# Optimization experiments

Measured on AMD Instinct MI355X. Metric: run time of the kernel, lower is better.

The kernel has to match this reference:

```python
import jax, jax.numpy as jnp
import numpy as np

N, D, DIN, S, R = 128, 2560, 5120, 16, 160  # users, d_model, d_inner, d_state, dt_rank


def setup_inputs() -> dict:
    key = jax.random.key(0)
    ks = jax.random.split(key, 16)
    f = lambda k, shape, s: jax.random.normal(k, shape, dtype=jnp.float32) * s
    return {
        "x": f(ks[0], (1, 1, N, D), 1.0),
        "conv_state0": f(ks[1], (1, 1, N, DIN), 0.1),
        "conv_state1": f(ks[2], (1, 1, N, DIN), 0.1),
        "conv_state2": f(ks[3], (1, 1, N, DIN), 0.1),
        "conv_state3": f(ks[4], (1, 1, N, DIN), 0.1),
        "ssm_state": f(ks[5], (N, DIN, S), 0.1),
        "ssm_proj": f(ks[6], (D, DIN), 0.02),
        "mlp_proj": f(ks[7], (D, DIN), 0.02),
        "down_proj": f(ks[8], (DIN, D), 0.02),
        "conv_w": f(ks[9], (4, DIN), 0.2),
        "conv_bias": f(ks[10], (DIN,), 0.1),
        "x_proj_w": f(ks[11], (DIN, R + 2 * S), 0.02),
        "dt_proj_w": f(ks[12], (R, DIN), 0.05),
        "dt_proj_b": f(ks[13], (DIN,), 0.1),
        "A_log": jnp.log(jnp.broadcast_to(jnp.arange(1, S + 1, dtype=jnp.float32), (DIN, S))),
        "D_param": jnp.ones((DIN,), jnp.float32),
    }


def reference(x, conv_state0, conv_state1, conv_state2, conv_state3, ssm_state,
              ssm_proj, mlp_proj, down_proj, conv_w, conv_bias,
              x_proj_w, dt_proj_w, dt_proj_b, A_log, D_param):
    r = dt_proj_w.shape[0]
    s = A_log.shape[1]
    x2 = x[0, 0]                         # (N, D)
    xs = x2 @ ssm_proj                   # (N, DIN) in_proj (ssm half)
    # shifted conv state window: oldest state (conv_state0) is dropped
    states = (conv_state1[0, 0], conv_state2[0, 0], conv_state3[0, 0], xs)
    conv_out = conv_bias + conv_w[0] * states[0] + conv_w[1] * states[1] \
        + conv_w[2] * states[2] + conv_w[3] * states[3]   # (N, DIN)
    u = jax.nn.silu(conv_out)
    # selective-scan single step (TtMambaSSM)
    proj = u @ x_proj_w                  # (N, R + 2S)
    dt = jax.nn.softplus(proj[:, :r] @ dt_proj_w + dt_proj_b)  # (N, DIN)
    Bm = proj[:, r:r + s]                # (N, S)
    Cm = proj[:, r + s:]                 # (N, S)
    A = -jnp.exp(A_log)                  # (DIN, S)
    dA = jnp.exp(dt[:, :, None] * A[None])                     # (N, DIN, S)
    h = dA * ssm_state + dt[:, :, None] * Bm[:, None, :] * u[:, :, None]
    y = jnp.einsum('nds,ns->nd', h, Cm) + D_param * u          # (N, DIN)
    # residual/gate branch and output projection (note: no silu on res, as in source)
    res = x2 @ mlp_proj                  # (N, DIN)
    out = (y * res) @ down_proj          # (N, D)
    return out[None, None]               # (1, 1, N, D)
```

## Files before the change

kernel.cpp:

```cpp
#include <hip/hip_runtime.h>

using u16 = unsigned short;
using u32 = unsigned int;

typedef __attribute__((ext_vector_type(8))) short short8;
typedef __attribute__((ext_vector_type(4))) float floatx4;

constexpr int TOKENS = 128;
constexpr int DM = 2560;
constexpr int DI = 5120;
constexpr int NS = 16;
constexpr int NR = 160;
constexpr int NP = 192;

constexpr size_t ND    = (size_t)TOKENS * DI;
constexpr size_t XS_P  = 0;
constexpr size_t RES_P = XS_P + 8 * ND;
constexpr size_t U_OFF = RES_P + 8 * ND;
constexpr size_t DT_P  = U_OFF + ND;
constexpr size_t PRJ_P = DT_P + 5 * ND;
constexpr size_t PRJ   = PRJ_P + 40 * (size_t)(TOKENS * NP);
constexpr size_t NEED  = PRJ + (size_t)(TOKENS * NP);

constexpr size_t S_XS  = 0;
constexpr size_t S_RES = S_XS + ND;
constexpr size_t S_U   = S_RES + ND;
constexpr size_t S_DT  = S_U + ND;
constexpr size_t S_PRJ = S_DT + ND;
constexpr size_t S_OAC = S_PRJ + (size_t)(TOKENS * NP);

__device__ __forceinline__ float bf2f(u16 h) {
  u32 u = ((u32)h) << 16;
  return __builtin_bit_cast(float, u);
}
__device__ __forceinline__ u16 f2bf(float f) {
  u32 u = __builtin_bit_cast(u32, f);
  u += 0x7FFFu + ((u >> 16) & 1u);
  return (u16)(u >> 16);
}
__device__ __forceinline__ u32 pk2(float a, float b) {
  u32 r;
  asm("v_cvt_pk_bf16_f32 %0, %1, %2" : "=v"(r) : "v"(a), "v"(b));
  return r;
}
__device__ __forceinline__ float ldsc(const void* p, size_t i, bool bf) {
  return bf ? bf2f(((const u16*)p)[i]) : ((const float*)p)[i];
}
__device__ __forceinline__ uint4 ld8(const void* p, size_t i, bool bf) {
  if (bf) return *(const uint4*)((const u16*)p + i);
  const float4* f = (const float4*)((const float*)p + i);
  float4 a = f[0], b = f[1];
  return (uint4){pk2(a.x, a.y), pk2(a.z, a.w), pk2(b.x, b.y), pk2(b.z, b.w)};
}
__device__ __forceinline__ void ld8f(const void* p, size_t i, bool bf, float* o) {
  if (bf) {
    uint4 v = *(const uint4*)((const u16*)p + i);
    const u16* h = (const u16*)&v;
#pragma unroll
    for (int e = 0; e < 8; e++) o[e] = bf2f(h[e]);
  } else {
    const float4* f = (const float4*)((const float*)p + i);
    float4 a = f[0], b = f[1];
    o[0] = a.x; o[1] = a.y; o[2] = a.z; o[3] = a.w;
    o[4] = b.x; o[5] = b.y; o[6] = b.z; o[7] = b.w;
  }
}

struct GemmP {
  const void* A; int lda; int a_ws;
  const void* B; const void* B2;
  float* C; float* C2;
  int ldb; int ldc;
  int ksteps;
  int nx_half;
  int atomic;
  size_t cstride;
  const u32* probe;
};

__global__ __launch_bounds__(256, 4) void gemm_k(GemmP p) {
  __shared__ __align__(16) u16 As[128 * 32];
  __shared__ __align__(16) u16 Bs[64 * 32];

  const bool bf = (p.probe[0] != 0u);
  const int tid = threadIdx.x;
  const int bx = blockIdx.x;
  const void* B = p.B; float* C = p.C;
  int nblk = bx;
  if (bx >= p.nx_half) { B = p.B2; C = p.C2; nblk = bx - p.nx_half; }
  const int n0 = nblk * 64;
  const int kstart = blockIdx.y * p.ksteps * 32;
  if (!p.atomic) C += blockIdx.y * p.cstride;

  const int wave = tid >> 6, lane = tid & 63;
  const int q = lane >> 4, l16 = lane & 15;
  const int wx = wave & 1, wy = wave >> 1;

  const bool a_f32 = p.a_ws || !bf;

  const int ac = tid & 3;
  const int am0 = tid >> 2;
  const bool bact = tid < 128;
  const int bc = tid & 7, pr = (tid >> 3) & 15;
  const int bn8 = bc * 8, k2 = 2 * pr;

  floatx4 acc[4][2];
#pragma unroll
  for (int mi = 0; mi < 4; mi++)
#pragma unroll
    for (int ni = 0; ni < 2; ni++) acc[mi][ni] = (floatx4){0.f, 0.f, 0.f, 0.f};

  auto load_tiles = [&](int ks, uint4* aO, uint4* bO) {
    const int kb = kstart + ks * 32;
#pragma unroll
    for (int pa = 0; pa < 2; pa++) {
      const int m = am0 + pa * 64;
      const size_t off = (size_t)m * p.lda + kb + ac * 8;
      if (!a_f32) {
        aO[pa] = *(const uint4*)((const u16*)p.A + off);
      } else {
        const float4* f = (const float4*)((const float*)p.A + off);
        float4 x0 = f[0], x1 = f[1];
        aO[pa] = (uint4){pk2(x0.x, x0.y), pk2(x0.z, x0.w),
                         pk2(x1.x, x1.y), pk2(x1.z, x1.w)};
      }
    }
    if (bact) {
      bO[0] = ld8(B, (size_t)(kb + k2) * p.ldb + n0 + bn8, bf);
      bO[1] = ld8(B, (size_t)(kb + k2 + 1) * p.ldb + n0 + bn8, bf);
    }
  };

  auto store_tiles = [&](const uint4* aO, const uint4* bO) {
#pragma unroll
    for (int pa = 0; pa < 2; pa++) {
      const int m = am0 + pa * 64;
      *(uint4*)&As[m * 32 + ((ac ^ (m & 3)) << 3)] = aO[pa];
    }
    if (bact) {
      const u16* lo = (const u16*)&bO[0];
      const u16* hi = (const u16*)&bO[1];
#pragma unroll
      for (int j = 0; j < 8; j++) {
        const int n = bn8 + j;
        const int blk = (k2 >> 3) ^ ((n ^ (n >> 3)) & 3);
        *(u32*)&Bs[n * 32 + (blk << 3) + (k2 & 7)] =
            (u32)lo[j] | ((u32)hi[j] << 16);
      }
    }
  };

  const int swA = l16 & 3;
  const int arow = (wy * 64 + l16) * 32;
  const int ao = ((q ^ swA) << 3);
  int nrow[2], bo[2];
#pragma unroll
  for (int ni = 0; ni < 2; ni++) {
    const int n = wx * 32 + ni * 16 + l16;
    nrow[ni] = n * 32;
    bo[ni] = ((q ^ ((n ^ (n >> 3)) & 3)) << 3);
  }

  auto compute = [&]() {
    short8 a[4];
#pragma unroll
    for (int mi = 0; mi < 4; mi++)
      a[mi] = __builtin_bit_cast(short8,
          *(const uint4*)&As[arow + mi * 16 * 32 + ao]);
    short8 b[2];
#pragma unroll
    for (int ni = 0; ni < 2; ni++)
      b[ni] = __builtin_bit_cast(short8, *(const uint4*)&Bs[nrow[ni] + bo[ni]]);
#pragma unroll
    for (int mi = 0; mi < 4; mi++)
#pragma unroll
      for (int ni = 0; ni < 2; ni++)
        acc[mi][ni] = __builtin_amdgcn_mfma_f32_16x16x32_bf16(
            a[mi], b[ni], acc[mi][ni], 0, 0, 0);
  };

  uint4 a0[2], b0[2], a1[2], b1[2];
  load_tiles(0, a0, b0);
  if (p.ksteps > 1) load_tiles(1, a1, b1);
  int ks = 0;
  for (;;) {
    __syncthreads();
    store_tiles(a0, b0);
    if (ks + 2 < p.ksteps) load_tiles(ks + 2, a0, b0);
    __syncthreads();
    compute();
    if (++ks == p.ksteps) break;

    __syncthreads();
    store_tiles(a1, b1);
    if (ks + 2 < p.ksteps) load_tiles(ks + 2, a1, b1);
    __syncthreads();
    compute();
    if (++ks == p.ksteps) break;
  }

#pragma unroll
  for (int ni = 0; ni < 2; ni++) {
    const int col = n0 + wx * 32 + ni * 16 + l16;
#pragma unroll
    for (int mi = 0; mi < 4; mi++) {
      floatx4 v = acc[mi][ni];
#pragma unroll
      for (int r = 0; r < 4; r++) {
        const int row = wy * 64 + mi * 16 + q * 4 + r;
        if (p.atomic) atomicAdd(&C[(size_t)row * p.ldc + col], v[r]);
        else          C[(size_t)row * p.ldc + col] = v[r];
      }
    }
  }
}

__global__ __launch_bounds__(256) void epi_u_k(
    const float* __restrict__ xs_p, int nred, size_t pstride,
    const void* __restrict__ cs1, const void* __restrict__ cs2,
    const void* __restrict__ cs3, const void* __restrict__ cw,
    const void* __restrict__ cb, float* __restrict__ u,
    const u32* __restrict__ probe) {
  const bool bf = (probe[0] != 0u);
  const int idx = blockIdx.x * 256 + threadIdx.x;
  const int n = idx / (DI / 8);
  const int d0 = (idx - n * (DI / 8)) * 8;
  const size_t nd = (size_t)n * DI + d0;
  float xv[8] = {0.f, 0.f, 0.f, 0.f, 0.f, 0.f, 0.f, 0.f};
  for (int j = 0; j < nred; j++) {
    const float4* f = (const float4*)(xs_p + j * pstride + nd);
    float4 a = f[0], b = f[1];
    xv[0] += a.x; xv[1] += a.y; xv[2] += a.z; xv[3] += a.w;
    xv[4] += b.x; xv[5] += b.y; xv[6] += b.z; xv[7] += b.w;
  }
  float c1[8], c2[8], c3[8], w0[8], w1[8], w2[8], w3[8], bb[8];
  ld8f(cs1, nd, bf, c1);
  ld8f(cs2, nd, bf, c2);
  ld8f(cs3, nd, bf, c3);
  ld8f(cw, (size_t)0 * DI + d0, bf, w0);
  ld8f(cw, (size_t)1 * DI + d0, bf, w1);
  ld8f(cw, (size_t)2 * DI + d0, bf, w2);
  ld8f(cw, (size_t)3 * DI + d0, bf, w3);
  ld8f(cb, d0, bf, bb);
  float o[8];
#pragma unroll
  for (int e = 0; e < 8; e++) {
    float cv = bb[e] + w0[e] * c1[e] + w1[e] * c2[e] + w2[e] * c3[e] +
               w3[e] * xv[e];
    o[e] = cv / (1.0f + __expf(-cv));
  }
  float4* uo = (float4*)(u + nd);
  uo[0] = (float4){o[0], o[1], o[2], o[3]};
  uo[1] = (float4){o[4], o[5], o[6], o[7]};
}

__global__ __launch_bounds__(256) void rproj_k(const float* __restrict__ in,
                                               int nred, size_t pstride,
                                               float* __restrict__ out) {
  const int i = blockIdx.x * 256 + threadIdx.x;
  if (i < TOKENS * NP) {
    float s = 0.f;
    for (int j = 0; j < nred; j++) s += in[j * pstride + i];
    out[i] = s;
  }
}

__global__ __launch_bounds__(256) void ssm_k(
    const void* __restrict__ sstate, const void* __restrict__ alog,
    const void* __restrict__ dparam, const void* __restrict__ dtb,
    const float* __restrict__ proj, const float* __restrict__ dt_p,
    int nred_d, size_t sd, const float* __restrict__ u,
    const float* __restrict__ res_p, int nred_r, size_t sr,
    float* __restrict__ z, const u32* __restrict__ probe) {
  const bool bf = (probe[0] != 0u);
  const int n = blockIdx.y;
  const int d = blockIdx.x * 256 + threadIdx.x;
  __shared__ float Bsh[NS], Csh[NS];
  if (threadIdx.x < NS)
    Bsh[threadIdx.x] = proj[(size_t)n * NP + NR + threadIdx.x];
  else if (threadIdx.x < 2 * NS)
    Csh[threadIdx.x - NS] = proj[(size_t)n * NP + NR + threadIdx.x];
  __syncthreads();
  const size_t nd = (size_t)n * DI + d;
  const float uv = u[nd];
  float rv = 0.f;
  for (int j = 0; j < nred_r; j++) rv += res_p[j * sr + nd];
  float sv = ldsc(dtb, d, bf);
  for (int j = 0; j < nred_d; j++) sv += dt_p[j * sd + nd];
  const float dtv = (sv > 20.0f) ? sv : log1pf(__expf(sv));

  float stf[16], alf[16];
  if (bf) {
    u16 st[16], al[16];
    const uint4* sp = (const uint4*)((const u16*)sstate + nd * 16);
    *(uint4*)&st[0] = sp[0]; *(uint4*)&st[8] = sp[1];
    const uint4* ap = (const uint4*)((const u16*)alog + (size_t)d * 16);
    *(uint4*)&al[0] = ap[0]; *(uint4*)&al[8] = ap[1];
#pragma unroll
    for (int s = 0; s < 16; s++) { stf[s] = bf2f(st[s]); alf[s] = bf2f(al[s]); }
  } else {
    const float4* sp = (const float4*)((const float*)sstate + nd * 16);
    const float4* ap = (const float4*)((const float*)alog + (size_t)d * 16);
#pragma unroll
    for (int i = 0; i < 4; i++) {
      float4 s4 = sp[i], a4 = ap[i];
      stf[i * 4 + 0] = s4.x; stf[i * 4 + 1] = s4.y; stf[i * 4 + 2] = s4.z; stf[i * 4 + 3] = s4.w;
      alf[i * 4 + 0] = a4.x; alf[i * 4 + 1] = a4.y; alf[i * 4 + 2] = a4.z; alf[i * 4 + 3] = a4.w;
    }
  }
  float y = 0.f;
#pragma unroll
  for (int s = 0; s < 16; s++) {
    float Aa = -__expf(alf[s]);
    float dA = __expf(dtv * Aa);
    float h = dA * stf[s] + dtv * Bsh[s] * uv;
    y += h * Csh[s];
  }
  y += ldsc(dparam, d, bf) * uv;
  z[nd] = y * rv;
}

__global__ __launch_bounds__(256) void cvt_k(const float* __restrict__ in,
                                             int nred, size_t pstride,
                                             void* __restrict__ out, int n,
                                             const u32* __restrict__ probe) {
  const bool bf = (probe[0] != 0u);
  const int i0 = (blockIdx.x * 256 + threadIdx.x) * 8;
  if (i0 + 8 <= n) {
    float o[8] = {0.f, 0.f, 0.f, 0.f, 0.f, 0.f, 0.f, 0.f};
    for (int j = 0; j < nred; j++) {
      const float4* f = (const float4*)(in + j * pstride + i0);
      float4 a = f[0], b = f[1];
      o[0] += a.x; o[1] += a.y; o[2] += a.z; o[3] += a.w;
      o[4] += b.x; o[5] += b.y; o[6] += b.z; o[7] += b.w;
    }
    if (bf) {
      uint4 v = {pk2(o[0], o[1]), pk2(o[2], o[3]), pk2(o[4], o[5]), pk2(o[6], o[7])};
      *(uint4*)((u16*)out + i0) = v;
    } else {
      float4* fo = (float4*)((float*)out + i0);
      fo[0] = (float4){o[0], o[1], o[2], o[3]};
      fo[1] = (float4){o[4], o[5], o[6], o[7]};
    }
  } else {
    for (int i = i0; i < n; i++) {
      float s = 0.f;
      for (int j = 0; j < nred; j++) s += in[j * pstride + i];
      if (bf) ((u16*)out)[i] = f2bf(s);
      else    ((float*)out)[i] = s;
    }
  }
}

extern "C" void kernel_launch(void* const* d_in, const int* in_sizes, int n_in,
                              void* d_out, int out_size, void* d_ws, size_t ws_size,
                              hipStream_t stream) {
  const void* x         = d_in[0];
  const void* cs1       = d_in[2];
  const void* cs2       = d_in[3];
  const void* cs3       = d_in[4];
  const void* ssm_state = d_in[5];
  const void* ssm_proj  = d_in[6];
  const void* mlp_proj  = d_in[7];
  const void* down_proj = d_in[8];
  const void* conv_w    = d_in[9];
  const void* conv_b    = d_in[10];
  const void* x_proj_w  = d_in[11];
  const void* dt_proj_w = d_in[12];
  const void* dt_proj_b = d_in[13];
  const void* A_log     = d_in[14];
  const void* D_param   = d_in[15];
  const u32*  probe     = (const u32*)A_log;

  float* ws = (float*)d_ws;
  const bool big = (ws_size / sizeof(float)) >= NEED;

  if (big) {
    float* xs_p  = ws + XS_P;
    float* res_p = ws + RES_P;
    float* u     = ws + U_OFF;
    float* dt_p  = ws + DT_P;
    float* prj_p = ws + PRJ_P;
    float* prj   = ws + PRJ;
    float* z     = ws + XS_P;
    float* oac_p = ws + RES_P;

    {
      GemmP p{};
      p.A = x; p.lda = DM; p.a_ws = 0;
      p.B = ssm_proj; p.B2 = mlp_proj;
      p.C = xs_p; p.C2 = res_p;
      p.ldb = DI; p.ldc = DI;
      p.ksteps = 10; p.nx_half = 80; p.atomic = 0; p.cstride = ND;
      p.probe = probe;
      gemm_k<<<dim3(160, 8), 256, 0, stream>>>(p);
    }
    epi_u_k<<<dim3(TOKENS * DI / 8 / 256), 256, 0, stream>>>(
        xs_p, 8, ND, cs1, cs2, cs3, conv_w, conv_b, u, probe);
    {
      GemmP p{};
      p.A = u; p.lda = DI; p.a_ws = 1;
      p.B = x_proj_w; p.B2 = nullptr;
      p.C = prj_p; p.C2 = nullptr;
      p.ldb = NP; p.ldc = NP;
      p.ksteps = 4; p.nx_half = 1 << 30; p.atomic = 0;
      p.cstride = (size_t)TOKENS * NP;
      p.probe = probe;
      gemm_k<<<dim3(3, 40), 256, 0, stream>>>(p);
    }
    rproj_k<<<dim3((TOKENS * NP + 255) / 256), 256, 0, stream>>>(
        prj_p, 40, (size_t)TOKENS * NP, prj);
    {
      GemmP p{};
      p.A = prj; p.lda = NP; p.a_ws = 1;
      p.B = dt_proj_w; p.B2 = nullptr;
      p.C = dt_p; p.C2 = nullptr;
      p.ldb = DI; p.ldc = DI;
      p.ksteps = 1; p.nx_half = 1 << 30; p.atomic = 0; p.cstride = ND;
      p.probe = probe;
      gemm_k<<<dim3(DI / 64, 5), 256, 0, stream>>>(p);
    }
    ssm_k<<<dim3(DI / 256, TOKENS), 256, 0, stream>>>(
        ssm_state, A_log, D_param, dt_proj_b, prj, dt_p, 5, ND, u,
        res_p, 8, ND, z, probe);
    {
      GemmP p{};
      p.A = z; p.lda = DI; p.a_ws = 1;
      p.B = down_proj; p.B2 = nullptr;
      p.C = oac_p; p.C2 = nullptr;
      p.ldb = DM; p.ldc = DM;
      p.ksteps = 10; p.nx_half = 1 << 30; p.atomic = 0;
      p.cstride = (size_t)TOKENS * DM;
      p.probe = probe;
      gemm_k<<<dim3(DM / 64, 16), 256, 0, stream>>>(p);
    }
    cvt_k<<<dim3((out_size / 8 + 255) / 256), 256, 0, stream>>>(
        oac_p, 16, (size_t)TOKENS * DM, d_out, out_size, probe);
  } else {
    float* xs  = ws + S_XS;
    float* res = ws + S_RES;
    float* u   = ws + S_U;
    float* dt  = ws + S_DT;
    float* prj = ws + S_PRJ;
    float* oac = ws + S_OAC;
    float* z   = ws + S_XS;

    hipMemsetAsync(xs,  0, ND * sizeof(float), stream);
    hipMemsetAsync(res, 0, ND * sizeof(float), stream);
    hipMemsetAsync(dt,  0, ND * sizeof(float), stream);
    hipMemsetAsync(prj, 0, (size_t)TOKENS * NP * sizeof(float), stream);
    hipMemsetAsync(oac, 0, (size_t)TOKENS * DM * sizeof(float), stream);

    {
      GemmP p{};
      p.A = x; p.lda = DM; p.a_ws = 0;
      p.B = ssm_proj; p.B2 = mlp_proj;
      p.C = xs; p.C2 = res;
      p.ldb = DI; p.ldc = DI;
      p.ksteps = 10; p.nx_half = 80; p.atomic = 1; p.cstride = 0;
      p.probe = probe;
      gemm_k<<<dim3(160, 8), 256, 0, stream>>>(p);
    }
    epi_u_k<<<dim3(TOKENS * DI / 8 / 256), 256, 0, stream>>>(
        xs, 1, 0, cs1, cs2, cs3, conv_w, conv_b, u, probe);
    {
      GemmP p{};
      p.A = u; p.lda = DI; p.a_ws = 1;
      p.B = x_proj_w; p.B2 = nullptr;
      p.C = prj; p.C2 = nullptr;
      p.ldb = NP; p.ldc = NP;
      p.ksteps = 4; p.nx_half = 1 << 30; p.atomic = 1; p.cstride = 0;
      p.probe = probe;
      gemm_k<<<dim3(3, 40), 256, 0, stream>>>(p);
    }
    {
      GemmP p{};
      p.A = prj; p.lda = NP; p.a_ws = 1;
      p.B = dt_proj_w; p.B2 = nullptr;
      p.C = dt; p.C2 = nullptr;
      p.ldb = DI; p.ldc = DI;
      p.ksteps = 1; p.nx_half = 1 << 30; p.atomic = 1; p.cstride = 0;
      p.probe = probe;
      gemm_k<<<dim3(DI / 64, 5), 256, 0, stream>>>(p);
    }
    ssm_k<<<dim3(DI / 256, TOKENS), 256, 0, stream>>>(
        ssm_state, A_log, D_param, dt_proj_b, prj, dt, 1, 0, u,
        res, 1, 0, z, probe);
    {
      GemmP p{};
      p.A = z; p.lda = DI; p.a_ws = 1;
      p.B = down_proj; p.B2 = nullptr;
      p.C = oac; p.C2 = nullptr;
      p.ldb = DM; p.ldc = DM;
      p.ksteps = 10; p.nx_half = 1 << 30; p.atomic = 1; p.cstride = 0;
      p.probe = probe;
      gemm_k<<<dim3(DM / 64, 16), 256, 0, stream>>>(p);
    }
    cvt_k<<<dim3((out_size / 8 + 255) / 256), 256, 0, stream>>>(
        oac, 1, 0, d_out, out_size, probe);
  }
}
```

Before: 340.5 us.

## Double-buffer GEMM LDS tiles with one barrier per step and fewer K splits

The GEMM kernel now keeps two LDS tile buffers, so storing the next tile and computing the current one need only a single barrier per k-step instead of two. Global loads now keep raw fp32 data in registers and convert to bf16 at store time, which delays the conversion instead of blocking right after the load. The split-K factor for the in-proj and down-proj GEMMs drops from 8/16 to 5/10 with more k-steps per block, which cuts the partial-sum traffic and the reduction work in the following kernels. The cost is double the LDS use, more live registers, and a lower occupancy hint (3 blocks instead of 4).

```diff
diff --git a/kernel.cpp b/kernel.cpp
--- a/kernel.cpp
+++ b/kernel.cpp
@@ -15,8 +15,8 @@
 
 constexpr size_t ND    = (size_t)TOKENS * DI;
 constexpr size_t XS_P  = 0;
-constexpr size_t RES_P = XS_P + 8 * ND;
-constexpr size_t U_OFF = RES_P + 8 * ND;
+constexpr size_t RES_P = XS_P + 5 * ND;
+constexpr size_t U_OFF = RES_P + 5 * ND;
 constexpr size_t DT_P  = U_OFF + ND;
 constexpr size_t PRJ_P = DT_P + 5 * ND;
 constexpr size_t PRJ   = PRJ_P + 40 * (size_t)(TOKENS * NP);
@@ -43,14 +43,12 @@
   asm("v_cvt_pk_bf16_f32 %0, %1, %2" : "=v"(r) : "v"(a), "v"(b));
   return r;
 }
+__device__ __forceinline__ uint4 pack8(uint4 lo, uint4 hi) {
+  float4 a = __builtin_bit_cast(float4, lo), b = __builtin_bit_cast(float4, hi);
+  return (uint4){pk2(a.x, a.y), pk2(a.z, a.w), pk2(b.x, b.y), pk2(b.z, b.w)};
+}
 __device__ __forceinline__ float ldsc(const void* p, size_t i, bool bf) {
   return bf ? bf2f(((const u16*)p)[i]) : ((const float*)p)[i];
-}
-__device__ __forceinline__ uint4 ld8(const void* p, size_t i, bool bf) {
-  if (bf) return *(const uint4*)((const u16*)p + i);
-  const float4* f = (const float4*)((const float*)p + i);
-  float4 a = f[0], b = f[1];
-  return (uint4){pk2(a.x, a.y), pk2(a.z, a.w), pk2(b.x, b.y), pk2(b.z, b.w)};
 }
 __device__ __forceinline__ void ld8f(const void* p, size_t i, bool bf, float* o) {
   if (bf) {
@@ -78,9 +76,9 @@
   const u32* probe;
 };
 
-__global__ __launch_bounds__(256, 4) void gemm_k(GemmP p) {
-  __shared__ __align__(16) u16 As[128 * 32];
-  __shared__ __align__(16) u16 Bs[64 * 32];
+__global__ __launch_bounds__(256, 3) void gemm_k(GemmP p) {
+  __shared__ __align__(16) u16 As[2 * 128 * 32];
+  __shared__ __align__(16) u16 Bs[2 * 64 * 32];
 
   const bool bf = (p.probe[0] != 0u);
   const int tid = threadIdx.x;
@@ -110,42 +108,59 @@
 #pragma unroll
     for (int ni = 0; ni < 2; ni++) acc[mi][ni] = (floatx4){0.f, 0.f, 0.f, 0.f};
 
-  auto load_tiles = [&](int ks, uint4* aO, uint4* bO) {
+  auto load_tiles = [&](int ks, uint4* ra, uint4* rb) {
     const int kb = kstart + ks * 32;
-#pragma unroll
-    for (int pa = 0; pa < 2; pa++) {
-      const int m = am0 + pa * 64;
-      const size_t off = (size_t)m * p.lda + kb + ac * 8;
-      if (!a_f32) {
-        aO[pa] = *(const uint4*)((const u16*)p.A + off);
+    if (!a_f32) {
+      ra[0] = *(const uint4*)((const u16*)p.A + (size_t)am0 * p.lda + kb + ac * 8);
+      ra[1] = *(const uint4*)((const u16*)p.A + (size_t)(am0 + 64) * p.lda + kb + ac * 8);
+    } else {
+      const float* Af = (const float*)p.A;
+      const float4* f0 = (const float4*)(Af + (size_t)am0 * p.lda + kb + ac * 8);
+      const float4* f1 = (const float4*)(Af + (size_t)(am0 + 64) * p.lda + kb + ac * 8);
+      ra[0] = __builtin_bit_cast(uint4, f0[0]); ra[1] = __builtin_bit_cast(uint4, f0[1]);
+      ra[2] = __builtin_bit_cast(uint4, f1[0]); ra[3] = __builtin_bit_cast(uint4, f1[1]);
+    }
+    if (bact) {
+      if (bf) {
+        rb[0] = *(const uint4*)((const u16*)B + (size_t)(kb + k2) * p.ldb + n0 + bn8);
+        rb[1] = *(const uint4*)((const u16*)B + (size_t)(kb + k2 + 1) * p.ldb + n0 + bn8);
       } else {
-        const float4* f = (const float4*)((const float*)p.A + off);
-        float4 x0 = f[0], x1 = f[1];
-        aO[pa] = (uint4){pk2(x0.x, x0.y), pk2(x0.z, x0.w),
-                         pk2(x1.x, x1.y), pk2(x1.z, x1.w)};
+        const float* Bf = (const float*)B;
+        const float4* g0 = (const float4*)(Bf + (size_t)(kb + k2) * p.ldb + n0 + bn8);
+        const float4* g1 = (const float4*)(Bf + (size_t)(kb + k2 + 1) * p.ldb + n0 + bn8);
+        rb[0] = __builtin_bit_cast(uint4, g0[0]); rb[1] = __builtin_bit_cast(uint4, g0[1]);
+        rb[2] = __builtin_bit_cast(uint4, g1[0]); rb[3] = __builtin_bit_cast(uint4, g1[1]);
       }
     }
+  };
+
+  auto store_tiles = [&](int b, const uint4* ra, const uint4* rb) {
+    u16* Ab = &As[b * 4096];
+    u16* Bb = &Bs[b * 2048];
+    uint4 w0, w1;
+    if (!a_f32) { w0 = ra[0]; w1 = ra[1]; }
+    else        { w0 = pack8(ra[0], ra[1]); w1 = pack8(ra[2], ra[3]); }
+    *(uint4*)&Ab[am0 * 32 + ((ac ^ (am0 & 3)) << 3)] = w0;
+    const int m1 = am0 + 64;
+    *(uint4*)&Ab[m1 * 32 + ((ac ^ (m1 & 3)) << 3)] = w1;
     if (bact) {
-      bO[0] = ld8(B, (size_t)(kb + k2) * p.ldb + n0 + bn8, bf);
-      bO[1] = ld8(B, (size_t)(kb + k2 + 1) * p.ldb + n0 + bn8, bf);
-    }
-  };
-
-  auto store_tiles = [&](const uint4* aO, const uint4* bO) {
-#pragma unroll
-    for (int pa = 0; pa < 2; pa++) {
-      const int m = am0 + pa * 64;
-      *(uint4*)&As[m * 32 + ((ac ^ (m & 3)) << 3)] = aO[pa];
-    }
-    if (bact) {
-      const u16* lo = (const u16*)&bO[0];
-      const u16* hi = (const u16*)&bO[1];
+      u32 pk[8];
+      if (bf) {
+        const u16* lo = (const u16*)&rb[0];
+        const u16* hi = (const u16*)&rb[1];
+#pragma unroll
+        for (int j = 0; j < 8; j++) pk[j] = (u32)lo[j] | ((u32)hi[j] << 16);
+      } else {
+        const float* lo = (const float*)&rb[0];
+        const float* hi = (const float*)&rb[2];
+#pragma unroll
+        for (int j = 0; j < 8; j++) pk[j] = pk2(lo[j], hi[j]);
+      }
 #pragma unroll
       for (int j = 0; j < 8; j++) {
         const int n = bn8 + j;
         const int blk = (k2 >> 3) ^ ((n ^ (n >> 3)) & 3);
-        *(u32*)&Bs[n * 32 + (blk << 3) + (k2 & 7)] =
-            (u32)lo[j] | ((u32)hi[j] << 16);
+        *(u32*)&Bb[n * 32 + (blk << 3) + (k2 & 7)] = pk[j];
       }
     }
   };
@@ -161,43 +176,48 @@
     bo[ni] = ((q ^ ((n ^ (n >> 3)) & 3)) << 3);
   }
 
-  auto compute = [&]() {
+  auto compute = [&](int b) {
+    const u16* Ab = &As[b * 4096];
+    const u16* Bb = &Bs[b * 2048];
     short8 a[4];
 #pragma unroll
     for (int mi = 0; mi < 4; mi++)
-      a[mi] = __builtin_bit_cast(short8,
-          *(const uint4*)&As[arow + mi * 16 * 32 + ao]);
-    short8 b[2];
+      a[mi] = __builtin_bit_cast(short8, *(const uint4*)&Ab[arow + mi * 512 + ao]);
+    short8 bb[2];
 #pragma unroll
     for (int ni = 0; ni < 2; ni++)
-      b[ni] = __builtin_bit_cast(short8, *(const uint4*)&Bs[nrow[ni] + bo[ni]]);
+      bb[ni] = __builtin_bit_cast(short8, *(const uint4*)&Bb[nrow[ni] + bo[ni]]);
 #pragma unroll
     for (int mi = 0; mi < 4; mi++)
 #pragma unroll
       for (int ni = 0; ni < 2; ni++)
         acc[mi][ni] = __builtin_amdgcn_mfma_f32_16x16x32_bf16(
-            a[mi], b[ni], acc[mi][ni], 0, 0, 0);
+            a[mi], bb[ni], acc[mi][ni], 0, 0, 0);
   };
 
-  uint4 a0[2], b0[2], a1[2], b1[2];
-  load_tiles(0, a0, b0);
-  if (p.ksteps > 1) load_tiles(1, a1, b1);
-  int ks = 0;
+#define FENCE_BAR()                                        \
+  asm volatile("s_waitcnt lgkmcnt(0)" ::: "memory");       \
+  __builtin_amdgcn_sched_barrier(0);                       \
+  __builtin_amdgcn_s_barrier()
+
+  uint4 ra0[4], rb0[4], ra1[4], rb1[4];
+  load_tiles(0, ra0, rb0);
+  if (p.ksteps > 1) load_tiles(1, ra1, rb1);
+  int t = 0;
   for (;;) {
-    __syncthreads();
-    store_tiles(a0, b0);
-    if (ks + 2 < p.ksteps) load_tiles(ks + 2, a0, b0);
-    __syncthreads();
-    compute();
-    if (++ks == p.ksteps) break;
-
-    __syncthreads();
-    store_tiles(a1, b1);
-    if (ks + 2 < p.ksteps) load_tiles(ks + 2, a1, b1);
-    __syncthreads();
-    compute();
-    if (++ks == p.ksteps) break;
-  }
+    store_tiles(0, ra0, rb0);
+    if (t + 2 < p.ksteps) load_tiles(t + 2, ra0, rb0);
+    FENCE_BAR();
+    compute(0);
+    if (++t == p.ksteps) break;
+
+    store_tiles(1, ra1, rb1);
+    if (t + 2 < p.ksteps) load_tiles(t + 2, ra1, rb1);
+    FENCE_BAR();
+    compute(1);
+    if (++t == p.ksteps) break;
+  }
+#undef FENCE_BAR
 
 #pragma unroll
   for (int ni = 0; ni < 2; ni++) {
@@ -391,12 +411,12 @@
       p.B = ssm_proj; p.B2 = mlp_proj;
       p.C = xs_p; p.C2 = res_p;
       p.ldb = DI; p.ldc = DI;
-      p.ksteps = 10; p.nx_half = 80; p.atomic = 0; p.cstride = ND;
-      p.probe = probe;
-      gemm_k<<<dim3(160, 8), 256, 0, stream>>>(p);
+      p.ksteps = 16; p.nx_half = 80; p.atomic = 0; p.cstride = ND;
+      p.probe = probe;
+      gemm_k<<<dim3(160, 5), 256, 0, stream>>>(p);
     }
     epi_u_k<<<dim3(TOKENS * DI / 8 / 256), 256, 0, stream>>>(
-        xs_p, 8, ND, cs1, cs2, cs3, conv_w, conv_b, u, probe);
+        xs_p, 5, ND, cs1, cs2, cs3, conv_w, conv_b, u, probe);
     {
       GemmP p{};
       p.A = u; p.lda = DI; p.a_ws = 1;
@@ -422,20 +442,20 @@
     }
     ssm_k<<<dim3(DI / 256, TOKENS), 256, 0, stream>>>(
         ssm_state, A_log, D_param, dt_proj_b, prj, dt_p, 5, ND, u,
-        res_p, 8, ND, z, probe);
+        res_p, 5, ND, z, probe);
     {
       GemmP p{};
       p.A = z; p.lda = DI; p.a_ws = 1;
       p.B = down_proj; p.B2 = nullptr;
       p.C = oac_p; p.C2 = nullptr;
       p.ldb = DM; p.ldc = DM;
-      p.ksteps = 10; p.nx_half = 1 << 30; p.atomic = 0;
+      p.ksteps = 16; p.nx_half = 1 << 30; p.atomic = 0;
       p.cstride = (size_t)TOKENS * DM;
       p.probe = probe;
-      gemm_k<<<dim3(DM / 64, 16), 256, 0, stream>>>(p);
+      gemm_k<<<dim3(DM / 64, 10), 256, 0, stream>>>(p);
     }
     cvt_k<<<dim3((out_size / 8 + 255) / 256), 256, 0, stream>>>(
-        oac_p, 16, (size_t)TOKENS * DM, d_out, out_size, probe);
+        oac_p, 10, (size_t)TOKENS * DM, d_out, out_size, probe);
   } else {
     float* xs  = ws + S_XS;
     float* res = ws + S_RES;
```

Result: faster. 314.3 us (-7.7%).
